# Performance work log

Hardware: AMD Instinct MI355X
Metric: run time of the kernel (lower is better)

Reference implementation:

```python
import jax, jax.numpy as jnp
import numpy as np

# Neighbor offsets (di, dj) implied by each 3x3 kernel: out_j = gray - shift(gray, di, dj)
# kernel0..kernel7 as defined in the torch module (center weight +1, one neighbor -1)
OFFSETS = [(0, -1), (1, -1), (1, 0), (1, 1), (0, 1), (-1, 1), (-1, 0), (-1, -1)]
EPS = 1e-5  # torch InstanceNorm2d default


def setup_inputs() -> dict:
    key = jax.random.key(0)
    x = jax.random.uniform(key, (8, 3, 1024, 1024), dtype=jnp.float32)
    return {"x": x}


def _ltpe(x):
    # RGB -> gray, [B,1,H,W]
    g = (0.3 * x[:, 0] + 0.59 * x[:, 1] + 0.11 * x[:, 2])[:, None]
    B, _, H, W = g.shape
    gp = jnp.pad(g, ((0, 0), (0, 0), (1, 1), (1, 1)))  # zero pad = conv padding=1
    out = jnp.zeros_like(g)
    for j, (di, dj) in enumerate(OFFSETS):
        nb = gp[:, :, 1 + di:1 + di + H, 1 + dj:1 + dj + W]
        d = (g - nb + 1.0) * 0.5          # (conv_out + 1) * 0.5
        out = out + d * (float(2 ** j) / 255.0)
    # InstanceNorm2d(1): per (b, c) mean/biased-var over spatial dims, no affine
    mean = jnp.mean(out, axis=(2, 3), keepdims=True)
    var = jnp.var(out, axis=(2, 3), keepdims=True)
    out = (out - mean) * jax.lax.rsqrt(var + EPS)
    return jnp.concatenate([out, out, out], axis=1)  # [B,3,H,W]


def reference(x):
    return _ltpe(x)
```

## Files before the change

### kernel.cpp

```cpp
#include <hip/hip_runtime.h>
#include <hip/hip_cooperative_groups.h>
#include <math.h>

namespace cg = cooperative_groups;

constexpr int H = 1024, W = 1024, B = 8;
constexpr int NPIX = H * W;

constexpr int FROWS = 8;
constexpr int FGRID = B * (H / FROWS);

__device__ __forceinline__ float grayat(const float* __restrict__ xb, int r, int c) {
    const float* p = xb + (size_t)r * W + c;
    return 0.3f * p[0] + 0.59f * p[NPIX] + 0.11f * p[2 * NPIX];
}

__global__ __launch_bounds__(256, 4)
void ltpe_fused(const float* __restrict__ x, float* __restrict__ out,
                float2* __restrict__ part)
{
    const int blk  = blockIdx.x;
    const int b    = blk & 7;
    const int g    = blk >> 3;
    const int r0   = g * FROWS;
    const int tid  = threadIdx.x;
    const int c    = tid << 2;
    const int lane = tid & 63;
    const float* xb = x + (size_t)b * 3 * NPIX;

    constexpr float w0 = 1.f/255.f,  w1 = 2.f/255.f,  w2 = 4.f/255.f,  w3 = 8.f/255.f,
                    w4 = 16.f/255.f, w5 = 32.f/255.f, w6 = 64.f/255.f, w7 = 128.f/255.f;

    auto grayrow = [&](int rr, float (&dst)[6]) {
        float4 q0 = {0.f,0.f,0.f,0.f}, q1 = q0, q2 = q0;
        const bool rok = (unsigned)rr < (unsigned)H;
        if (rok) {
            const float* p = xb + (size_t)rr * W + c;
            q0 = *reinterpret_cast<const float4*>(p);
            q1 = *reinterpret_cast<const float4*>(p + NPIX);
            q2 = *reinterpret_cast<const float4*>(p + 2 * NPIX);
        }
        float4 gq;
        gq.x = 0.3f * q0.x + 0.59f * q1.x + 0.11f * q2.x;
        gq.y = 0.3f * q0.y + 0.59f * q1.y + 0.11f * q2.y;
        gq.z = 0.3f * q0.z + 0.59f * q1.z + 0.11f * q2.z;
        gq.w = 0.3f * q0.w + 0.59f * q1.w + 0.11f * q2.w;
        float l  = __shfl_up(gq.w, 1);
        float rt = __shfl_down(gq.x, 1);
        if (lane == 0)  l  = (c > 0 && rok)     ? grayat(xb, rr, c - 1) : 0.f;
        if (lane == 63) rt = (c + 4 < W && rok) ? grayat(xb, rr, c + 4) : 0.f;
        dst[0] = l; dst[1] = gq.x; dst[2] = gq.y; dst[3] = gq.z; dst[4] = gq.w; dst[5] = rt;
    };

    float gray[3][6];
    float4 tq[FROWS];
    float s = 0.f, ss = 0.f;

    #pragma unroll
    for (int i = 0; i < FROWS + 2; ++i) {
        grayrow(r0 - 1 + i, gray[i % 3]);
        if (i >= 2) {
            const float (&up)[6] = gray[(i - 2) % 3];
            const float (&mi)[6] = gray[(i - 1) % 3];
            const float (&dn)[6] = gray[i % 3];
            float tv[4];
            #pragma unroll
            for (int kk = 0; kk < 4; ++kk) {
                float sv = w0 * mi[kk];
                sv = fmaf(w1, dn[kk],     sv);
                sv = fmaf(w2, dn[kk + 1], sv);
                sv = fmaf(w3, dn[kk + 2], sv);
                sv = fmaf(w4, mi[kk + 2], sv);
                sv = fmaf(w5, up[kk + 2], sv);
                sv = fmaf(w6, up[kk + 1], sv);
                sv = fmaf(w7, up[kk],     sv);
                tv[kk] = 0.5f * mi[kk + 1] + 0.5f - 0.5f * sv;
                s += tv[kk];
                ss = fmaf(tv[kk], tv[kk], ss);
            }
            tq[i - 2] = make_float4(tv[0], tv[1], tv[2], tv[3]);
        }
    }

    #pragma unroll
    for (int off = 32; off >= 1; off >>= 1) {
        s  += __shfl_down(s, off);
        ss += __shfl_down(ss, off);
    }
    __shared__ float2 wred[4];
    if (lane == 0) wred[tid >> 6] = make_float2(s, ss);
    __syncthreads();
    if (tid == 0) {
        float2 a0 = wred[0], a1 = wred[1], a2 = wred[2], a3 = wred[3];
        part[(size_t)b * 128 + g] = make_float2(a0.x + a1.x + a2.x + a3.x,
                                                a0.y + a1.y + a2.y + a3.y);
    }

    cg::this_grid().sync();

    const float4* pp = reinterpret_cast<const float4*>(part + (size_t)b * 128);
    const float4 u = pp[lane];
    double ds = (double)u.x + (double)u.z;
    double dss = (double)u.y + (double)u.w;
    #pragma unroll
    for (int off = 1; off <= 32; off <<= 1) {
        ds  += __shfl_xor(ds, off);
        dss += __shfl_xor(dss, off);
    }
    const double n    = (double)NPIX;
    const double dmean = ds / n;
    const double dvar  = dss / n - dmean * dmean;
    const float mean = (float)dmean;
    const float rstd = (float)(1.0 / sqrt(dvar + 1e-5));

    float* ob = out + (size_t)b * 3 * NPIX + (size_t)r0 * W + c;
    #pragma unroll
    for (int rr = 0; rr < FROWS; ++rr) {
        const float4 t4 = tq[rr];
        float4 y;
        y.x = (t4.x - mean) * rstd;
        y.y = (t4.y - mean) * rstd;
        y.z = (t4.z - mean) * rstd;
        y.w = (t4.w - mean) * rstd;
        float* p = ob + (size_t)rr * W;
        *reinterpret_cast<float4*>(p)            = y;
        *reinterpret_cast<float4*>(p + NPIX)     = y;
        *reinterpret_cast<float4*>(p + 2 * NPIX) = y;
    }
}

constexpr int ROWS = 2;
constexpr int RG   = H / ROWS;

__device__ __forceinline__ void gload_lds16(const float* g, float* l) {
    __builtin_amdgcn_global_load_lds(
        (const __attribute__((address_space(1))) void*)g,
        (__attribute__((address_space(3))) void*)l, 16, 0, 0);
}

__global__ __launch_bounds__(256)
void ltpe_stage1(const float* __restrict__ x, float* __restrict__ out,
                 float2* __restrict__ part)
{
    __shared__ float lds[4][3][W];
    const int b   = blockIdx.y;
    const int k   = blockIdx.x;
    const int kg  = ((k & 7) << 6) | (k >> 3);
    const int r0  = kg * ROWS;
    const int tid = threadIdx.x;
    const int w   = tid >> 6;
    const int l   = tid & 63;
    const int c   = tid << 2;
    const float* xb = x + (size_t)b * 3 * NPIX;

    #pragma unroll
    for (int s = 0; s < 4; ++s) {
        const int rr = r0 - 1 + s;
        if ((unsigned)rr < (unsigned)H) {
            #pragma unroll
            for (int ch = 0; ch < 3; ++ch) {
                const float* gp = xb + (size_t)ch * NPIX + (size_t)rr * W + (w << 8) + (l << 2);
                gload_lds16(gp, &lds[s][ch][w << 8]);
            }
        } else {
            const float4 z = make_float4(0.f, 0.f, 0.f, 0.f);
            #pragma unroll
            for (int ch = 0; ch < 3; ++ch)
                *reinterpret_cast<float4*>(&lds[s][ch][c]) = z;
        }
    }
    __syncthreads();

    const int ql = (tid == 0)   ? 0   : tid - 1;
    const int qr = (tid == 255) ? 255 : tid + 1;
    float g6[4][6];
    #pragma unroll
    for (int s = 0; s < 4; ++s) {
        const float4 o0 = *reinterpret_cast<const float4*>(&lds[s][0][c]);
        const float4 o1 = *reinterpret_cast<const float4*>(&lds[s][1][c]);
        const float4 o2 = *reinterpret_cast<const float4*>(&lds[s][2][c]);
        const float4 l0 = *reinterpret_cast<const float4*>(&lds[s][0][ql << 2]);
        const float4 l1 = *reinterpret_cast<const float4*>(&lds[s][1][ql << 2]);
        const float4 l2 = *reinterpret_cast<const float4*>(&lds[s][2][ql << 2]);
        const float4 rq0 = *reinterpret_cast<const float4*>(&lds[s][0][qr << 2]);
        const float4 rq1 = *reinterpret_cast<const float4*>(&lds[s][1][qr << 2]);
        const float4 rq2 = *reinterpret_cast<const float4*>(&lds[s][2][qr << 2]);
        g6[s][1] = 0.3f * o0.x + 0.59f * o1.x + 0.11f * o2.x;
        g6[s][2] = 0.3f * o0.y + 0.59f * o1.y + 0.11f * o2.y;
        g6[s][3] = 0.3f * o0.z + 0.59f * o1.z + 0.11f * o2.z;
        g6[s][4] = 0.3f * o0.w + 0.59f * o1.w + 0.11f * o2.w;
        g6[s][0] = (tid == 0)   ? 0.f : 0.3f * l0.w  + 0.59f * l1.w  + 0.11f * l2.w;
        g6[s][5] = (tid == 255) ? 0.f : 0.3f * rq0.x + 0.59f * rq1.x + 0.11f * rq2.x;
    }

    constexpr float w0 = 1.f/255.f,  w1 = 2.f/255.f,  w2 = 4.f/255.f,  w3 = 8.f/255.f,
                    w4 = 16.f/255.f, w5 = 32.f/255.f, w6 = 64.f/255.f, w7 = 128.f/255.f;
    float s = 0.f, ss = 0.f;
    float* ob = out + (size_t)b * 3 * NPIX + (size_t)r0 * W + c;
    #pragma unroll
    for (int rr = 0; rr < ROWS; ++rr) {
        const float (&up)[6] = g6[rr];
        const float (&mi)[6] = g6[rr + 1];
        const float (&dn)[6] = g6[rr + 2];
        float tv[4];
        #pragma unroll
        for (int kk = 0; kk < 4; ++kk) {
            float sv = w0 * mi[kk];
            sv = fmaf(w1, dn[kk],     sv);
            sv = fmaf(w2, dn[kk + 1], sv);
            sv = fmaf(w3, dn[kk + 2], sv);
            sv = fmaf(w4, mi[kk + 2], sv);
            sv = fmaf(w5, up[kk + 2], sv);
            sv = fmaf(w6, up[kk + 1], sv);
            sv = fmaf(w7, up[kk],     sv);
            tv[kk] = 0.5f * mi[kk + 1] + 0.5f - 0.5f * sv;
            s += tv[kk];
            ss = fmaf(tv[kk], tv[kk], ss);
        }
        float4 t4 = {tv[0], tv[1], tv[2], tv[3]};
        *reinterpret_cast<float4*>(ob + (size_t)rr * W) = t4;
    }

    #pragma unroll
    for (int off = 32; off >= 1; off >>= 1) {
        s  += __shfl_down(s, off);
        ss += __shfl_down(ss, off);
    }
    __shared__ float2 wred[4];
    if (l == 0) wred[w] = make_float2(s, ss);
    __syncthreads();
    if (tid == 0) {
        float2 a0 = wred[0], a1 = wred[1], a2 = wred[2], a3 = wred[3];
        part[(size_t)b * RG + kg] = make_float2(a0.x + a1.x + a2.x + a3.x,
                                                a0.y + a1.y + a2.y + a3.y);
    }
}

__global__ __launch_bounds__(256)
void ltpe_stageB(float* __restrict__ out, const float2* __restrict__ part)
{
    const int b    = blockIdx.y;
    const int r    = blockIdx.x;
    const int tid  = threadIdx.x;
    const int lane = tid & 63;

    const float4* pp = reinterpret_cast<const float4*>(part + (size_t)b * RG);
    const float4 u = pp[tid];
    double s  = (double)u.x + (double)u.z;
    double ss = (double)u.y + (double)u.w;
    #pragma unroll
    for (int off = 32; off >= 1; off >>= 1) {
        s  += __shfl_down(s, off);
        ss += __shfl_down(ss, off);
    }
    __shared__ double red[8];
    __shared__ float2 mv;
    const int wv = tid >> 6;
    if (lane == 0) { red[wv] = s; red[4 + wv] = ss; }
    __syncthreads();
    if (tid == 0) {
        const double S  = red[0] + red[1] + red[2] + red[3];
        const double SS = red[4] + red[5] + red[6] + red[7];
        const double n    = (double)NPIX;
        const double mean = S / n;
        const double var  = SS / n - mean * mean;
        mv = make_float2((float)mean, (float)(1.0 / sqrt(var + 1e-5)));
    }
    __syncthreads();
    const float mean = mv.x, rstd = mv.y;

    const size_t base = (size_t)b * 3 * NPIX + (size_t)r * W + (tid << 2);
    const float4 t4 = *reinterpret_cast<const float4*>(out + base);
    float4 y;
    y.x = (t4.x - mean) * rstd;
    y.y = (t4.y - mean) * rstd;
    y.z = (t4.z - mean) * rstd;
    y.w = (t4.w - mean) * rstd;
    *reinterpret_cast<float4*>(out + base)            = y;
    *reinterpret_cast<float4*>(out + base + NPIX)     = y;
    *reinterpret_cast<float4*>(out + base + 2 * NPIX) = y;
}

extern "C" void kernel_launch(void* const* d_in, const int* in_sizes, int n_in,
                              void* d_out, int out_size, void* d_ws, size_t ws_size,
                              hipStream_t stream)
{
    const float* x = (const float*)d_in[0];
    float* out = (float*)d_out;
    float2* part = (float2*)d_ws;

    int nb = 0;
    hipError_t qe = hipOccupancyMaxActiveBlocksPerMultiprocessor(
        &nb, reinterpret_cast<const void*>(ltpe_fused), 256, 0);

    if (qe == hipSuccess && nb * 256 >= FGRID) {
        void* args[] = { (void*)&x, (void*)&out, (void*)&part };
        hipLaunchCooperativeKernel((void*)ltpe_fused, dim3(FGRID), dim3(256),
                                   args, 0, stream);
    } else {
        ltpe_stage1<<<dim3(RG, B), 256, 0, stream>>>(x, out, part);
        ltpe_stageB<<<dim3(H, B), 256, 0, stream>>>(out, part);
    }
}
```

Measured before the change: 51.15 us.

## Pipeline fused kernel row loads through LDS with async global_load_lds ring

The cooperative fused kernel now has each block handle 16 rows instead of 8, which halves the grid to 512 blocks and relaxes launch bounds to 2 waves per SIMD. Input rows are prefetched into a per-wave 5-slot LDS ring with direct global-to-LDS loads and explicit vmcnt waits, so loads overlap with the stencil math. Edge-column gray values are precomputed up front by the boundary lanes. This aims to hide memory latency in the single-pass kernel, at the cost of more registers per thread (16 float4 held for the second phase), fewer resident blocks, and fragile hand-tuned waitcnt counts.

```diff
diff --git a/kernel.cpp b/kernel.cpp
--- a/kernel.cpp
+++ b/kernel.cpp
@@ -7,107 +7,164 @@
 constexpr int H = 1024, W = 1024, B = 8;
 constexpr int NPIX = H * W;
 
-constexpr int FROWS = 8;
-constexpr int FGRID = B * (H / FROWS);
-
+constexpr int FR    = 16;
+constexpr int GPB   = H / FR;
+constexpr int FGRID = B * GPB;
+
+__device__ __forceinline__ void gload16(const float* g, float* l) {
+    __builtin_amdgcn_global_load_lds(
+        (const __attribute__((address_space(1))) void*)g,
+        (__attribute__((address_space(3))) void*)l, 16, 0, 0);
+}
 __device__ __forceinline__ float grayat(const float* __restrict__ xb, int r, int c) {
     const float* p = xb + (size_t)r * W + c;
     return 0.3f * p[0] + 0.59f * p[NPIX] + 0.11f * p[2 * NPIX];
 }
 
-__global__ __launch_bounds__(256, 4)
+__global__ __launch_bounds__(256, 2)
 void ltpe_fused(const float* __restrict__ x, float* __restrict__ out,
                 float2* __restrict__ part)
 {
+    __shared__ float lds[4][5][3][256];
+    __shared__ float2 wred[4];
+
     const int blk  = blockIdx.x;
     const int b    = blk & 7;
     const int g    = blk >> 3;
-    const int r0   = g * FROWS;
+    const int r0   = g * FR;
     const int tid  = threadIdx.x;
+    const int w    = tid >> 6;
+    const int lane = tid & 63;
     const int c    = tid << 2;
-    const int lane = tid & 63;
     const float* xb = x + (size_t)b * 3 * NPIX;
+    float (*ldsw)[3][256] = lds[w];
 
     constexpr float w0 = 1.f/255.f,  w1 = 2.f/255.f,  w2 = 4.f/255.f,  w3 = 8.f/255.f,
                     w4 = 16.f/255.f, w5 = 32.f/255.f, w6 = 64.f/255.f, w7 = 128.f/255.f;
 
-    auto grayrow = [&](int rr, float (&dst)[6]) {
-        float4 q0 = {0.f,0.f,0.f,0.f}, q1 = q0, q2 = q0;
-        const bool rok = (unsigned)rr < (unsigned)H;
-        if (rok) {
-            const float* p = xb + (size_t)rr * W + c;
-            q0 = *reinterpret_cast<const float4*>(p);
-            q1 = *reinterpret_cast<const float4*>(p + NPIX);
-            q2 = *reinterpret_cast<const float4*>(p + 2 * NPIX);
+    float pL[FR + 2], pR[FR + 2];
+    #pragma unroll
+    for (int i = 0; i < FR + 2; ++i) { pL[i] = 0.f; pR[i] = 0.f; }
+    if (lane == 0 && c > 0) {
+        #pragma unroll
+        for (int i = 0; i < FR + 2; ++i) {
+            const int rr = r0 - 1 + i;
+            if ((unsigned)rr < (unsigned)H) pL[i] = grayat(xb, rr, c - 1);
         }
-        float4 gq;
-        gq.x = 0.3f * q0.x + 0.59f * q1.x + 0.11f * q2.x;
-        gq.y = 0.3f * q0.y + 0.59f * q1.y + 0.11f * q2.y;
-        gq.z = 0.3f * q0.z + 0.59f * q1.z + 0.11f * q2.z;
-        gq.w = 0.3f * q0.w + 0.59f * q1.w + 0.11f * q2.w;
-        float l  = __shfl_up(gq.w, 1);
-        float rt = __shfl_down(gq.x, 1);
-        if (lane == 0)  l  = (c > 0 && rok)     ? grayat(xb, rr, c - 1) : 0.f;
-        if (lane == 63) rt = (c + 4 < W && rok) ? grayat(xb, rr, c + 4) : 0.f;
-        dst[0] = l; dst[1] = gq.x; dst[2] = gq.y; dst[3] = gq.z; dst[4] = gq.w; dst[5] = rt;
+    }
+    if (lane == 63 && c + 4 < W) {
+        #pragma unroll
+        for (int i = 0; i < FR + 2; ++i) {
+            const int rr = r0 - 1 + i;
+            if ((unsigned)rr < (unsigned)H) pR[i] = grayat(xb, rr, c + 4);
+        }
+    }
+    __builtin_amdgcn_sched_barrier(0);
+
+    auto stage = [&](int off, int slot) {
+        int rr = r0 - 1 + off;
+        rr = rr < 0 ? 0 : (rr > H - 1 ? H - 1 : rr);
+        const float* gp = xb + (size_t)rr * W + (w << 8) + (lane << 2);
+        gload16(gp,            &ldsw[slot][0][0]);
+        gload16(gp + NPIX,     &ldsw[slot][1][0]);
+        gload16(gp + 2*NPIX,   &ldsw[slot][2][0]);
     };
 
-    float gray[3][6];
-    float4 tq[FROWS];
+    auto grayc = [&](int off, int slot, float (&d)[6]) {
+        const bool rok = (unsigned)(r0 - 1 + off) < (unsigned)H;
+        const float4 a = *reinterpret_cast<const float4*>(&ldsw[slot][0][lane << 2]);
+        const float4 e = *reinterpret_cast<const float4*>(&ldsw[slot][1][lane << 2]);
+        const float4 f = *reinterpret_cast<const float4*>(&ldsw[slot][2][lane << 2]);
+        float g1 = 0.3f*a.x + 0.59f*e.x + 0.11f*f.x;
+        float g2 = 0.3f*a.y + 0.59f*e.y + 0.11f*f.y;
+        float g3 = 0.3f*a.z + 0.59f*e.z + 0.11f*f.z;
+        float g4 = 0.3f*a.w + 0.59f*e.w + 0.11f*f.w;
+        float glv = __shfl_up(g4, 1);
+        float grv = __shfl_down(g1, 1);
+        if (lane == 0)  glv = pL[off];
+        if (lane == 63) grv = pR[off];
+        if (!rok) { g1 = g2 = g3 = g4 = glv = grv = 0.f; }
+        d[0]=glv; d[1]=g1; d[2]=g2; d[3]=g3; d[4]=g4; d[5]=grv;
+    };
+
+    float gr6[3][6];
+    float4 tq[FR];
     float s = 0.f, ss = 0.f;
 
-    #pragma unroll
-    for (int i = 0; i < FROWS + 2; ++i) {
-        grayrow(r0 - 1 + i, gray[i % 3]);
-        if (i >= 2) {
-            const float (&up)[6] = gray[(i - 2) % 3];
-            const float (&mi)[6] = gray[(i - 1) % 3];
-            const float (&dn)[6] = gray[i % 3];
-            float tv[4];
-            #pragma unroll
-            for (int kk = 0; kk < 4; ++kk) {
-                float sv = w0 * mi[kk];
-                sv = fmaf(w1, dn[kk],     sv);
-                sv = fmaf(w2, dn[kk + 1], sv);
-                sv = fmaf(w3, dn[kk + 2], sv);
-                sv = fmaf(w4, mi[kk + 2], sv);
-                sv = fmaf(w5, up[kk + 2], sv);
-                sv = fmaf(w6, up[kk + 1], sv);
-                sv = fmaf(w7, up[kk],     sv);
-                tv[kk] = 0.5f * mi[kk + 1] + 0.5f - 0.5f * sv;
-                s += tv[kk];
-                ss = fmaf(tv[kk], tv[kk], ss);
-            }
-            tq[i - 2] = make_float4(tv[0], tv[1], tv[2], tv[3]);
-        }
-    }
+    stage(0, 0); stage(1, 1); stage(2, 2); stage(3, 3);
+    asm volatile("s_waitcnt vmcnt(6)" ::: "memory");
+    __builtin_amdgcn_sched_barrier(0);
+    grayc(0, 0, gr6[0]);
+    grayc(1, 1, gr6[1]);
+
+#define LTPE_STEP(I, WAITSTR)                                                  \
+    {                                                                          \
+        if ((I) + 4 <= FR + 1) stage((I) + 4, ((I) + 4) % 5);                  \
+        asm volatile(WAITSTR ::: "memory");                                    \
+        __builtin_amdgcn_sched_barrier(0);                                     \
+        grayc((I) + 2, ((I) + 2) % 5, gr6[((I) + 2) % 3]);                     \
+        const float (&up)[6] = gr6[(I) % 3];                                   \
+        const float (&mi)[6] = gr6[((I) + 1) % 3];                             \
+        const float (&dn)[6] = gr6[((I) + 2) % 3];                             \
+        float tv[4];                                                           \
+        _Pragma("unroll")                                                      \
+        for (int kk = 0; kk < 4; ++kk) {                                       \
+            float sv = w0 * mi[kk];                                            \
+            sv = fmaf(w1, dn[kk],     sv);                                     \
+            sv = fmaf(w2, dn[kk + 1], sv);                                     \
+            sv = fmaf(w3, dn[kk + 2], sv);                                     \
+            sv = fmaf(w4, mi[kk + 2], sv);                                     \
+            sv = fmaf(w5, up[kk + 2], sv);                                     \
+            sv = fmaf(w6, up[kk + 1], sv);                                     \
+            sv = fmaf(w7, up[kk],     sv);                                     \
+            tv[kk] = 0.5f * mi[kk + 1] + 0.5f - 0.5f * sv;                     \
+            s += tv[kk];                                                       \
+            ss = fmaf(tv[kk], tv[kk], ss);                                     \
+        }                                                                      \
+        tq[I] = make_float4(tv[0], tv[1], tv[2], tv[3]);                       \
+    }
+
+    LTPE_STEP(0,  "s_waitcnt vmcnt(6)")
+    LTPE_STEP(1,  "s_waitcnt vmcnt(6)")
+    LTPE_STEP(2,  "s_waitcnt vmcnt(6)")
+    LTPE_STEP(3,  "s_waitcnt vmcnt(6)")
+    LTPE_STEP(4,  "s_waitcnt vmcnt(6)")
+    LTPE_STEP(5,  "s_waitcnt vmcnt(6)")
+    LTPE_STEP(6,  "s_waitcnt vmcnt(6)")
+    LTPE_STEP(7,  "s_waitcnt vmcnt(6)")
+    LTPE_STEP(8,  "s_waitcnt vmcnt(6)")
+    LTPE_STEP(9,  "s_waitcnt vmcnt(6)")
+    LTPE_STEP(10, "s_waitcnt vmcnt(6)")
+    LTPE_STEP(11, "s_waitcnt vmcnt(6)")
+    LTPE_STEP(12, "s_waitcnt vmcnt(6)")
+    LTPE_STEP(13, "s_waitcnt vmcnt(6)")
+    LTPE_STEP(14, "s_waitcnt vmcnt(3)")
+    LTPE_STEP(15, "s_waitcnt vmcnt(0)")
+#undef LTPE_STEP
 
     #pragma unroll
     for (int off = 32; off >= 1; off >>= 1) {
         s  += __shfl_down(s, off);
         ss += __shfl_down(ss, off);
     }
-    __shared__ float2 wred[4];
-    if (lane == 0) wred[tid >> 6] = make_float2(s, ss);
+    if (lane == 0) wred[w] = make_float2(s, ss);
     __syncthreads();
     if (tid == 0) {
         float2 a0 = wred[0], a1 = wred[1], a2 = wred[2], a3 = wred[3];
-        part[(size_t)b * 128 + g] = make_float2(a0.x + a1.x + a2.x + a3.x,
+        part[(size_t)b * GPB + g] = make_float2(a0.x + a1.x + a2.x + a3.x,
                                                 a0.y + a1.y + a2.y + a3.y);
     }
 
     cg::this_grid().sync();
 
-    const float4* pp = reinterpret_cast<const float4*>(part + (size_t)b * 128);
-    const float4 u = pp[lane];
-    double ds = (double)u.x + (double)u.z;
-    double dss = (double)u.y + (double)u.w;
-    #pragma unroll
-    for (int off = 1; off <= 32; off <<= 1) {
-        ds  += __shfl_xor(ds, off);
-        dss += __shfl_xor(dss, off);
-    }
-    const double n    = (double)NPIX;
+    const float2 pv = part[(size_t)b * GPB + lane];
+    double ds = (double)pv.x, dss = (double)pv.y;
+    #pragma unroll
+    for (int o = 1; o <= 32; o <<= 1) {
+        ds  += __shfl_xor(ds, o);
+        dss += __shfl_xor(dss, o);
+    }
+    const double n     = (double)NPIX;
     const double dmean = ds / n;
     const double dvar  = dss / n - dmean * dmean;
     const float mean = (float)dmean;
@@ -115,14 +172,14 @@
 
     float* ob = out + (size_t)b * 3 * NPIX + (size_t)r0 * W + c;
     #pragma unroll
-    for (int rr = 0; rr < FROWS; ++rr) {
-        const float4 t4 = tq[rr];
+    for (int i = 0; i < FR; ++i) {
+        const float4 t4 = tq[i];
         float4 y;
         y.x = (t4.x - mean) * rstd;
         y.y = (t4.y - mean) * rstd;
         y.z = (t4.z - mean) * rstd;
         y.w = (t4.w - mean) * rstd;
-        float* p = ob + (size_t)rr * W;
+        float* p = ob + (size_t)i * W;
         *reinterpret_cast<float4*>(p)            = y;
         *reinterpret_cast<float4*>(p + NPIX)     = y;
         *reinterpret_cast<float4*>(p + 2 * NPIX) = y;
@@ -131,12 +188,6 @@
 
 constexpr int ROWS = 2;
 constexpr int RG   = H / ROWS;
-
-__device__ __forceinline__ void gload_lds16(const float* g, float* l) {
-    __builtin_amdgcn_global_load_lds(
-        (const __attribute__((address_space(1))) void*)g,
-        (__attribute__((address_space(3))) void*)l, 16, 0, 0);
-}
 
 __global__ __launch_bounds__(256)
 void ltpe_stage1(const float* __restrict__ x, float* __restrict__ out,
@@ -160,7 +211,7 @@
             #pragma unroll
             for (int ch = 0; ch < 3; ++ch) {
                 const float* gp = xb + (size_t)ch * NPIX + (size_t)rr * W + (w << 8) + (l << 2);
-                gload_lds16(gp, &lds[s][ch][w << 8]);
+                gload16(gp, &lds[s][ch][w << 8]);
             }
         } else {
             const float4 z = make_float4(0.f, 0.f, 0.f, 0.f);
```

Result: no change. 50.89 us (-0.5%).
